# Kernel optimization log

Measured on AMD Instinct MI355X. Metric: run time of the kernel, lower is better.

## Reference

```python
import jax, jax.numpy as jnp
import numpy as np

BN_EPS = 1e-5
BN_SCALE = 1.0 / np.sqrt(1.0 + BN_EPS).astype(np.float32)  # running_mean=0, running_var=1


def _conv1x1(x, w, b=None):
    y = jnp.einsum('bchw,oc->bohw', x, w)
    if b is not None:
        y = y + b.reshape(1, -1, 1, 1)
    return y


def _bn(x, g, b):
    # eval-mode BN with running_mean=0, running_var=1
    return x * (BN_SCALE * g).reshape(1, -1, 1, 1) + b.reshape(1, -1, 1, 1)


def _spatial_attn(x, w, b):
    avg = jnp.mean(x, axis=1, keepdims=True)
    mx = jnp.max(x, axis=1, keepdims=True)
    s = jnp.concatenate([avg, mx], axis=1)  # [B,2,H,W]
    y = jax.lax.conv_general_dilated(s, w, (1, 1), [(3, 3), (3, 3)],
                                     dimension_numbers=('NCHW', 'OIHW', 'NCHW'))
    return jax.nn.sigmoid(y + b.reshape(1, -1, 1, 1))  # [B,1,H,W]


def _channel_attn(x, w1, b1, w2, b2):
    avg = jnp.mean(x, axis=(2, 3))  # [B,C]
    mx = jnp.max(x, axis=(2, 3))
    fc = lambda v: jax.nn.relu(v @ w1.T + b1) @ w2.T + b2
    return jax.nn.sigmoid(fc(avg) + fc(mx))[:, :, None, None]  # [B,C,1,1]


def setup_inputs() -> dict:
    key = jax.random.key(0)
    B, C, H, W = 8, 256, 48, 48
    Cr, Cm = C // 8, C // 16
    ks = iter(jax.random.split(key, 24))
    n = lambda shape, scale=0.05: jax.random.normal(next(ks), shape, jnp.float32) * scale
    return dict(
        rgb=jax.random.normal(next(ks), (B, C, H, W), jnp.float32),
        chm=jax.random.normal(next(ks), (B, C, H, W), jnp.float32),
        rgb_sa_w=n((1, 2, 7, 7)), rgb_sa_b=jnp.zeros((1,), jnp.float32),
        chm_sa_w=n((1, 2, 7, 7)), chm_sa_b=jnp.zeros((1,), jnp.float32),
        rgb_fc1_w=n((Cm, C)), rgb_fc1_b=jnp.zeros((Cm,), jnp.float32),
        rgb_fc2_w=n((C, Cm)), rgb_fc2_b=jnp.zeros((C,), jnp.float32),
        chm_fc1_w=n((Cm, C)), chm_fc1_b=jnp.zeros((Cm,), jnp.float32),
        chm_fc2_w=n((C, Cm)), chm_fc2_b=jnp.zeros((C,), jnp.float32),
        rq_w=n((Cr, C)), rq_b=jnp.zeros((Cr,), jnp.float32),
        rk_w=n((Cr, C)), rk_b=jnp.zeros((Cr,), jnp.float32),
        rv_w=n((C, C)), rv_b=jnp.zeros((C,), jnp.float32),
        dq_w=n((Cr, C)), dq_b=jnp.zeros((Cr,), jnp.float32),
        dk_w=n((Cr, C)), dk_b=jnp.zeros((Cr,), jnp.float32),
        dv_w=n((C, C)), dv_b=jnp.zeros((C,), jnp.float32),
        gate_w=n((C, 2 * C)), gate_b=jnp.zeros((C,), jnp.float32),
        mlp1_w=n((24, C)), mlp1_g=jnp.ones((24,), jnp.float32), mlp1_b=jnp.zeros((24,), jnp.float32),
        mlp2_w=n((1, 24)), mlp2_g=jnp.ones((1,), jnp.float32), mlp2_b=jnp.zeros((1,), jnp.float32),
    )


def reference(rgb, chm, rgb_sa_w, rgb_sa_b, chm_sa_w, chm_sa_b,
              rgb_fc1_w, rgb_fc1_b, rgb_fc2_w, rgb_fc2_b,
              chm_fc1_w, chm_fc1_b, chm_fc2_w, chm_fc2_b,
              rq_w, rq_b, rk_w, rk_b, rv_w, rv_b,
              dq_w, dq_b, dk_w, dk_b, dv_w, dv_b,
              gate_w, gate_b, mlp1_w, mlp1_g, mlp1_b, mlp2_w, mlp2_g, mlp2_b):
    B, C, H, W = rgb.shape
    N = H * W
    Cr = rq_w.shape[0]
    scale = Cr ** -0.5

    # channel / spatial attentions
    rgb_sa = _spatial_attn(rgb, rgb_sa_w, rgb_sa_b)
    chm_sa = _spatial_attn(chm, chm_sa_w, chm_sa_b)
    rgb_ca = _channel_attn(rgb, rgb_fc1_w, rgb_fc1_b, rgb_fc2_w, rgb_fc2_b)
    chm_ca = _channel_attn(chm, chm_fc1_w, chm_fc1_b, chm_fc2_w, chm_fc2_b)

    attn_rgb = rgb * chm_sa * chm_ca
    attn_chm = chm * rgb_sa * rgb_ca

    # CAWF dual cross-modal attention
    flat = lambda x: x.reshape(B, -1, N)
    rq = flat(_conv1x1(rgb, rq_w, rq_b))   # [B,Cr,N]
    rk = flat(_conv1x1(rgb, rk_w, rk_b))
    rv = flat(_conv1x1(rgb, rv_w, rv_b))   # [B,C,N]
    dq = flat(_conv1x1(chm, dq_w, dq_b))
    dk = flat(_conv1x1(chm, dk_w, dk_b))
    dv = flat(_conv1x1(chm, dv_w, dv_b))

    rgb_attn = jax.nn.softmax(jnp.einsum('bcn,bcm->bnm', rq, dk) * scale, axis=-1)  # [B,N,N]
    chm_attn = jax.nn.softmax(jnp.einsum('bcn,bcm->bnm', dq, rk) * scale, axis=-1)
    rgb_att = jnp.einsum('bcn,bnm->bcm', rv, rgb_attn).reshape(B, C, H, W)
    chm_att = jnp.einsum('bcn,bnm->bcm', dv, chm_attn).reshape(B, C, H, W)

    c = jnp.concatenate([rgb_att, chm_att], axis=1)
    g = jax.nn.sigmoid(_conv1x1(c, gate_w, gate_b))
    c_fused = rgb_att * g + chm_att * (1.0 - g)
    d_fused = rgb_att * chm_att
    output = c_fused + d_fused

    h = jax.nn.relu(_bn(_conv1x1(output, mlp1_w), mlp1_g, mlp1_b))
    h = jax.nn.sigmoid(_bn(_conv1x1(h, mlp2_w), mlp2_g, mlp2_b))
    weight = jax.nn.sigmoid(h)  # double sigmoid as in original mlp (ConvBNSig + nn.Sigmoid)

    return attn_rgb + attn_chm * weight
```

## Files before the change

### kernel.cpp

```cpp
#include <hip/hip_runtime.h>
#include <hip/hip_bf16.h>
#include <cstdint>

#define DI __device__ __forceinline__

typedef float f32x4 __attribute__((ext_vector_type(4)));
typedef short bf16x8 __attribute__((ext_vector_type(8)));
typedef unsigned short u16x4 __attribute__((ext_vector_type(4)));

constexpr int B_ = 8, C_ = 256, HH = 48, WW = 48, N_ = 2304, CR = 32;
constexpr float QK_SCALE = 0.17677669529663687f;
constexpr float BN_SC = 0.99999500003749968f;

constexpr size_t QK_SZ   = (size_t)B_*N_*CR*2;
constexpr size_t V_SZ    = (size_t)B_*C_*N_*2;
constexpr size_t OFF_RQT = 0;
constexpr size_t OFF_RKT = OFF_RQT + QK_SZ;
constexpr size_t OFF_DQT = OFF_RKT + QK_SZ;
constexpr size_t OFF_DKT = OFF_DQT + QK_SZ;
constexpr size_t OFF_RV  = OFF_DKT + QK_SZ;
constexpr size_t OFF_DV  = OFF_RV + V_SZ;
constexpr size_t OFF_ATT = OFF_DV + V_SZ;
constexpr size_t ATT_SZ  = 2ull*B_*C_*N_*2;
constexpr size_t OFF_PCS = OFF_ATT;
constexpr size_t OFF_PCM = OFF_ATT + 2ull*8*36*256*4;
constexpr size_t OFF_FUSED = OFF_RV;
constexpr size_t OFF_SCONV = OFF_ATT + ATT_SZ;
constexpr size_t SCONV_SZ  = 2ull*B_*2*N_*4;
constexpr size_t OFF_SA    = OFF_SCONV + SCONV_SZ;
constexpr size_t SA_SZ     = 2ull*B_*N_*4;
constexpr size_t OFF_CAVG  = OFF_SA + SA_SZ;
constexpr size_t CST_SZ    = 2ull*B_*C_*4;
constexpr size_t OFF_CMAX  = OFF_CAVG + CST_SZ;
constexpr size_t OFF_CA    = OFF_CMAX + CST_SZ;
constexpr size_t OFF_WMAP  = OFF_CA + CST_SZ;
constexpr size_t OFF_WPROJ = OFF_WMAP + (size_t)B_*N_*4;
constexpr size_t WPROJ_SZ  = 2ull*320*256*2;
constexpr size_t OFF_WGATE = OFF_WPROJ + WPROJ_SZ;
constexpr size_t WS_NEEDED = OFF_WGATE + 256ull*512*2;

DI float bf2f(unsigned short u){ union{unsigned int i; float f;} v; v.i = ((unsigned int)u)<<16; return v.f; }
DI unsigned short f2bf(float f){ union{float f; unsigned int i;} v; v.f=f; unsigned int r = v.i + 0x7fffu + ((v.i>>16)&1u); return (unsigned short)(r>>16); }
DI float sigm(float x){ return 1.0f/(1.0f+__expf(-x)); }
DI u16x4 pk4(float p0, float p1, float p2, float p3){
  union { __hip_bfloat162 h[2]; u16x4 v; } u;
  u.h[0] = __float22bfloat162_rn(make_float2(p0, p1));
  u.h[1] = __float22bfloat162_rn(make_float2(p2, p3));
  return u.v;
}

__global__ void k_prep_w(const float* rq_w, const float* rk_w, const float* rv_w,
                         const float* dq_w, const float* dk_w, const float* dv_w,
                         const float* gate_w, unsigned short* wproj, unsigned short* wgate){
  int i = blockIdx.x*256 + threadIdx.x;
  if (i < 163840){
    int mod = i / 81920, r = (i >> 8) % 320, c = i & 255;
    const float* q = mod ? dq_w : rq_w;
    const float* k = mod ? dk_w : rk_w;
    const float* v = mod ? dv_w : rv_w;
    float val = (r < 32) ? q[r*256+c] : (r < 64 ? k[(r-32)*256+c] : v[(r-64)*256+c]);
    wproj[i] = f2bf(val);
  } else {
    int j = i - 163840;
    if (j < 131072) wgate[j] = f2bf(gate_w[j]);
  }
}

__global__ __launch_bounds__(256, 2) void k_redfuse(const float* rgb, const float* chm,
                                                    float* sconv, float* pcs, float* pcm){
  int mod = blockIdx.y;
  int b = blockIdx.x / 36, nt = blockIdx.x % 36;
  int pix0 = nt*64;
  const float* X = (mod ? chm : rgb) + (size_t)b*C_*N_ + pix0;
  __shared__ float xt[128][65];
  __shared__ float ls[4][64], lm[4][64];
  int t = threadIdx.x;
  int p = t & 63, cg = t >> 6;
  int srow0 = t >> 4, scol = (t & 15)*4;
  float s = 0.f, mx = -INFINITY;
  float* pcsb = pcs + ((size_t)(mod*8+b)*36 + nt)*256;
  float* pcmb = pcm + ((size_t)(mod*8+b)*36 + nt)*256;
  for (int half = 0; half < 2; ++half){
    __syncthreads();
    #pragma unroll
    for (int rr = 0; rr < 8; ++rr){
      int row = rr*16 + srow0;
      float4 v = *(const float4*)(X + (size_t)(half*128 + row)*N_ + scol);
      xt[row][scol] = v.x; xt[row][scol+1] = v.y; xt[row][scol+2] = v.z; xt[row][scol+3] = v.w;
    }
    __syncthreads();
    #pragma unroll 8
    for (int cc = 0; cc < 32; ++cc){
      float v = xt[cg*32 + cc][p];
      s += v; mx = fmaxf(mx, v);
    }
    if (t < 128){
      float cs = 0.f, cm = -INFINITY;
      #pragma unroll 8
      for (int pp = 0; pp < 64; ++pp){
        float v = xt[t][pp];
        cs += v; cm = fmaxf(cm, v);
      }
      pcsb[half*128 + t] = cs;
      pcmb[half*128 + t] = cm;
    }
  }
  ls[cg][p] = s; lm[cg][p] = mx;
  __syncthreads();
  if (cg == 0){
    s = ls[0][p]+ls[1][p]+ls[2][p]+ls[3][p];
    mx = fmaxf(fmaxf(lm[0][p],lm[1][p]), fmaxf(lm[2][p],lm[3][p]));
    sconv[((size_t)(mod*B_+b)*2 + 0)*N_ + pix0+p] = s*(1.f/256.f);
    sconv[((size_t)(mod*B_+b)*2 + 1)*N_ + pix0+p] = mx;
  }
}

__global__ void k_red_combine(const float* pcs, const float* pcm, float* cavg, float* cmax){
  int mod = blockIdx.x >> 3, b = blockIdx.x & 7, c = threadIdx.x;
  float s = 0.f, mx = -INFINITY;
  for (int nt = 0; nt < 36; ++nt){
    s += pcs[((size_t)(mod*8+b)*36 + nt)*256 + c];
    mx = fmaxf(mx, pcm[((size_t)(mod*8+b)*36 + nt)*256 + c]);
  }
  cavg[(mod*B_+b)*C_ + c] = s*(1.f/(float)N_);
  cmax[(mod*B_+b)*C_ + c] = mx;
}

__global__ void k_sa_ca(const float* sconv, const float* rgb_sa_w, const float* rgb_sa_b,
                        const float* chm_sa_w, const float* chm_sa_b, float* sa,
                        const float* cavg, const float* cmax,
                        const float* rw1, const float* rb1, const float* rw2, const float* rb2,
                        const float* cw1, const float* cb1, const float* cw2, const float* cb2,
                        float* ca){
  int x = blockIdx.x;
  if (x < 144){
    int mod = x / 72;
    int idx = (x % 72)*256 + threadIdx.x;
    int b = idx / N_, pix = idx % N_;
    int y = pix / WW, xx0 = pix % WW;
    const float* w7 = mod ? chm_sa_w : rgb_sa_w;
    float acc = (mod ? chm_sa_b : rgb_sa_b)[0];
    const float* sin0 = sconv + (size_t)(mod*B_+b)*2*N_;
    #pragma unroll
    for (int ic = 0; ic < 2; ++ic)
      for (int ky = 0; ky < 7; ++ky){
        int yy = y + ky - 3; if (yy < 0 || yy >= HH) continue;
        for (int kx = 0; kx < 7; ++kx){
          int xx = xx0 + kx - 3; if (xx < 0 || xx >= WW) continue;
          acc += w7[(ic*7+ky)*7+kx] * sin0[ic*N_ + yy*WW + xx];
        }
      }
    sa[(mod*B_+b)*N_ + pix] = sigm(acc);
  } else {
    int y = x - 144;
    int mod = y >> 3, b = y & 7;
    const float* w1 = mod ? cw1 : rw1;  const float* b1 = mod ? cb1 : rb1;
    const float* w2 = mod ? cw2 : rw2;  const float* b2 = mod ? cb2 : rb2;
    __shared__ float va[256], vm[256], h1a[16], h1m[16];
    int t = threadIdx.x;
    va[t] = cavg[(mod*B_+b)*C_ + t];
    vm[t] = cmax[(mod*B_+b)*C_ + t];
    __syncthreads();
    if (t < 32){
      int j = t & 15;
      const float* v = (t >= 16) ? vm : va;
      float s = b1[j];
      for (int c = 0; c < 256; ++c) s += w1[j*256+c]*v[c];
      float* hp = (t >= 16) ? h1m : h1a;
      hp[j] = fmaxf(s, 0.f);
    }
    __syncthreads();
    float fa = b2[t], fm = b2[t];
    #pragma unroll
    for (int j = 0; j < 16; ++j){ fa += w2[t*16+j]*h1a[j]; fm += w2[t*16+j]*h1m[j]; }
    ca[(mod*B_+b)*C_ + t] = sigm(fa + fm);
  }
}

__global__ __launch_bounds__(256, 2) void k_proj(
                       const float* rgb, const float* chm, const unsigned short* wproj,
                       const float* rq_b, const float* rk_b, const float* rv_b,
                       const float* dq_b, const float* dk_b, const float* dv_b,
                       unsigned short* wsu){
  int mod = blockIdx.z, b = blockIdx.y;
  int pix0 = blockIdx.x * 64;
  const float* X = (mod ? chm : rgb) + (size_t)b*C_*N_;
  const unsigned short* Wm = wproj + (size_t)mod*320*256;
  int lane = threadIdx.x & 63, w = threadIdx.x >> 6;
  int l15 = lane & 15, g = lane >> 4;
  __shared__ unsigned short xs[32*68];
  int srow = threadIdx.x >> 3, scol = (threadIdx.x & 7)*8;
  f32x4 acc[5][4];
  #pragma unroll
  for (int i = 0; i < 5; ++i)
    #pragma unroll
    for (int j = 0; j < 4; ++j) acc[i][j] = 0.f;
  for (int k0 = 0; k0 < 256; k0 += 32){
    const float* sp = X + (size_t)(k0 + srow)*N_ + pix0 + scol;
    float4 v0 = *(const float4*)sp;
    float4 v1 = *(const float4*)(sp + 4);
    u16x4 h0 = { f2bf(v0.x), f2bf(v0.y), f2bf(v0.z), f2bf(v0.w) };
    u16x4 h1 = { f2bf(v1.x), f2bf(v1.y), f2bf(v1.z), f2bf(v1.w) };
    __syncthreads();
    *(u16x4*)(xs + srow*68 + scol) = h0;
    *(u16x4*)(xs + srow*68 + scol + 4) = h1;
    __syncthreads();
    bf16x8 af[5];
    #pragma unroll
    for (int cf = 0; cf < 5; ++cf)
      af[cf] = *(const bf16x8*)(Wm + (size_t)(w*80 + cf*16 + l15)*256 + k0 + g*8);
    bf16x8 bx[4];
    #pragma unroll
    for (int mf = 0; mf < 4; ++mf)
      #pragma unroll
      for (int j = 0; j < 8; ++j)
        bx[mf][j] = (short)xs[(g*8+j)*68 + mf*16 + l15];
    #pragma unroll
    for (int cf = 0; cf < 5; ++cf)
      #pragma unroll
      for (int mf = 0; mf < 4; ++mf)
        acc[cf][mf] = __builtin_amdgcn_mfma_f32_16x16x32_bf16(af[cf], bx[mf], acc[cf][mf], 0, 0, 0);
  }
  const float* qb = mod ? dq_b : rq_b;
  const float* kb = mod ? dk_b : rk_b;
  const float* vb = mod ? dv_b : rv_b;
  unsigned short* qT = wsu + (mod ? OFF_DQT : OFF_RQT)/2;
  unsigned short* kT = wsu + (mod ? OFF_DKT : OFF_RKT)/2;
  unsigned short* vB = wsu + (mod ? OFF_DV  : OFF_RV )/2;
  #pragma unroll
  for (int cf = 0; cf < 5; ++cf){
    int base = w*80 + cf*16;
    #pragma unroll
    for (int mf = 0; mf < 4; ++mf){
      int col = pix0 + mf*16 + l15;
      if (base < 32){
        int o4 = base + g*4;
        u16x4 pk = { f2bf(acc[cf][mf][0] + qb[o4]),   f2bf(acc[cf][mf][1] + qb[o4+1]),
                     f2bf(acc[cf][mf][2] + qb[o4+2]), f2bf(acc[cf][mf][3] + qb[o4+3]) };
        *(u16x4*)(qT + (size_t)(b*N_ + col)*32 + o4) = pk;
      } else if (base < 64){
        int o4 = base - 32 + g*4;
        u16x4 pk = { f2bf(acc[cf][mf][0] + kb[o4]),   f2bf(acc[cf][mf][1] + kb[o4+1]),
                     f2bf(acc[cf][mf][2] + kb[o4+2]), f2bf(acc[cf][mf][3] + kb[o4+3]) };
        *(u16x4*)(kT + (size_t)(b*N_ + col)*32 + o4) = pk;
      } else {
        #pragma unroll
        for (int r = 0; r < 4; ++r){
          int o = base - 64 + g*4 + r;
          vB[((size_t)b*C_ + o)*N_ + col] = f2bf(acc[cf][mf][r] + vb[o]);
        }
      }
    }
  }
}

__global__ void k_phase_a(unsigned short* wsu){
  int orig = blockIdx.x;
  int b = orig & 7;
  int logical = orig >> 3;
  int a = logical / 36;
  int nb0 = (logical % 36)*64;
  int lane = threadIdx.x & 63, w = threadIdx.x >> 6;
  int l15 = lane & 15, g = lane >> 4;
  int n0 = nb0 + w*16;
  const unsigned short* Q = wsu + (a ? OFF_DQT : OFF_RQT)/2;
  const unsigned short* K = wsu + (a ? OFF_RKT : OFF_DKT)/2;
  bf16x8 af = *(const bf16x8*)(Q + (size_t)(b*N_ + n0 + l15)*32 + g*8);
  float lrun[4] = {0.f,0.f,0.f,0.f};
  for (int m0 = 0; m0 < N_; m0 += 64){
    f32x4 d[4];
    #pragma unroll
    for (int s = 0; s < 4; ++s){
      bf16x8 bk = *(const bf16x8*)(K + (size_t)(b*N_ + m0 + s*16 + l15)*32 + g*8);
      f32x4 z = 0.f;
      d[s] = __builtin_amdgcn_mfma_f32_16x16x32_bf16(af, bk, z, 0, 0, 0);
    }
    #pragma unroll
    for (int r = 0; r < 4; ++r)
      lrun[r] += (__expf(d[0][r]*QK_SCALE)+__expf(d[1][r]*QK_SCALE))
               + (__expf(d[2][r]*QK_SCALE)+__expf(d[3][r]*QK_SCALE));
  }
  #pragma unroll
  for (int r = 0; r < 4; ++r)
    #pragma unroll
    for (int msk = 1; msk < 16; msk <<= 1) lrun[r] += __shfl_xor(lrun[r], msk);
  __shared__ float lsv[64];
  if (l15 == 0){
    #pragma unroll
    for (int r = 0; r < 4; ++r) lsv[w*16 + g*4 + r] = 1.0f / lrun[r];
  }
  __syncthreads();
  unsigned short* V = wsu + (a ? OFF_DV : OFF_RV)/2 + ((size_t)b*C_ + threadIdx.x)*N_ + nb0;
  #pragma unroll
  for (int j8 = 0; j8 < 8; ++j8){
    bf16x8 vv = *(const bf16x8*)(V + j8*8);
    bf16x8 ov;
    #pragma unroll
    for (int e = 0; e < 8; ++e)
      ov[e] = (short)f2bf(bf2f((unsigned short)vv[e]) * lsv[j8*8 + e]);
    *(bf16x8*)(V + j8*8) = ov;
  }
}

__global__ __launch_bounds__(256, 3) void k_pv5(
                          const unsigned short* wsu, unsigned short* att){
  int orig = blockIdx.x;
  int logical = (orig & 7)*72 + (orig >> 3);
  int pair = logical / 36, mblk = logical % 36;
  int a = pair >> 3, b = pair & 7;
  int m0 = mblk*64;
  int lane = threadIdx.x & 63, w = threadIdx.x >> 6;
  int l15 = lane & 15, g = lane >> 4;
  int qm  = (w & 1)*32;
  int qnn = (w >> 1)*64;
  const unsigned short* Q = wsu + (a ? OFF_DQT : OFF_RQT)/2;
  const unsigned short* K = wsu + (a ? OFF_RKT : OFF_DKT)/2;
  const unsigned short* V = wsu + (a ? OFF_DV  : OFF_RV )/2;
  __shared__ __align__(16) unsigned char plds[2][64*256];

  bf16x8 kb[2];
  #pragma unroll
  for (int s = 0; s < 2; ++s)
    kb[s] = *(const bf16x8*)(K + (size_t)(b*N_ + m0 + qm + s*16 + l15)*32 + g*8);

  f32x4 acc[4][4];
  #pragma unroll
  for (int i = 0; i < 4; ++i)
    #pragma unroll
    for (int j = 0; j < 4; ++j) acc[i][j] = 0.f;

  auto computePh = [&](int n0base, int buf, int half){
    #pragma unroll
    for (int fi = 0; fi < 2; ++fi){
      int fr = half*2 + fi;
      int nb = n0base + qnn + fr*16;
      bf16x8 qa = *(const bf16x8*)(Q + (size_t)(b*N_ + nb + l15)*32 + g*8);
      #pragma unroll
      for (int fm = 0; fm < 2; ++fm){
        f32x4 z = 0.f;
        f32x4 d = __builtin_amdgcn_mfma_f32_16x16x32_bf16(qa, kb[fm], z, 0, 0, 0);
        int ml = qm + fm*16 + l15;
        int nl = qnn + fr*16 + g*4;
        u16x4 pk = pk4(__expf(d[0]*QK_SCALE), __expf(d[1]*QK_SCALE),
                       __expf(d[2]*QK_SCALE), __expf(d[3]*QK_SCALE));
        *(u16x4*)(plds[buf] + ml*256 + ((nl*2) ^ ((ml&7)<<4))) = pk;
      }
    }
  };

  computePh(0, 0, 0);
  computePh(0, 0, 1);
  __syncthreads();
  for (int t = 0; t < 18; ++t){
    int n0 = t*128;
    const unsigned char* pbuf = plds[t & 1];
    #pragma unroll
    for (int s = 0; s < 4; ++s){
      bf16x8 pb[4];
      #pragma unroll
      for (int mf = 0; mf < 4; ++mf){
        int ml = mf*16 + l15;
        pb[mf] = *(const bf16x8*)(pbuf + ml*256 + ((s*64 + g*16) ^ ((ml&7)<<4)));
      }
      bf16x8 av[4];
      #pragma unroll
      for (int cf = 0; cf < 4; ++cf)
        av[cf] = *(const bf16x8*)(V + ((size_t)b*C_ + w*64 + cf*16 + l15)*N_ + n0 + s*32 + g*8);
      if (t < 17 && s < 2) computePh(n0 + 128, (t+1)&1, s);
      __builtin_amdgcn_s_setprio(1);
      #pragma unroll
      for (int cf = 0; cf < 4; ++cf)
        #pragma unroll
        for (int mf = 0; mf < 4; ++mf)
          acc[cf][mf] = __builtin_amdgcn_mfma_f32_16x16x32_bf16(av[cf], pb[mf], acc[cf][mf], 0, 0, 0);
      __builtin_amdgcn_s_setprio(0);
    }
    __syncthreads();
  }
  unsigned short* ap = att + (((size_t)a*8 + b)*256)*N_;
  #pragma unroll
  for (int cf = 0; cf < 4; ++cf)
    #pragma unroll
    for (int mf = 0; mf < 4; ++mf)
      #pragma unroll
      for (int r = 0; r < 4; ++r){
        int c = w*64 + cf*16 + g*4 + r;
        int m = m0 + mf*16 + l15;
        ap[(size_t)c*N_ + m] = f2bf(acc[cf][mf][r]);
      }
}

__global__ __launch_bounds__(256, 2) void k_gatefuse(
                           const unsigned short* att, const unsigned short* wgate,
                           const float* gate_b, unsigned short* fused){
  int b = blockIdx.y, m0 = blockIdx.x*32;
  int lane = threadIdx.x & 63, w = threadIdx.x >> 6;
  int l15 = lane & 15, g = lane >> 4;
  __shared__ unsigned short ats[32][520];
  int row8 = threadIdx.x >> 3;
  int mq = (threadIdx.x & 7)*4;
  for (int rb = 0; rb < 16; ++rb){
    int k = rb*32 + row8;
    int aa = k >> 8, c = k & 255;
    size_t base = (((size_t)aa*8 + b)*256 + c)*N_ + m0 + mq;
    u16x4 p0 = *(const u16x4*)(att + base);
    #pragma unroll
    for (int j = 0; j < 4; ++j) ats[mq + j][k] = p0[j];
  }
  __syncthreads();
  f32x4 acc[4][2];
  #pragma unroll
  for (int i = 0; i < 4; ++i){ acc[i][0] = 0.f; acc[i][1] = 0.f; }
  for (int k0 = 0; k0 < 512; k0 += 32){
    bf16x8 aw[4], bt[2];
    #pragma unroll
    for (int of = 0; of < 4; ++of)
      aw[of] = *(const bf16x8*)(wgate + (size_t)(w*64 + of*16 + l15)*512 + k0 + g*8);
    #pragma unroll
    for (int mf = 0; mf < 2; ++mf)
      bt[mf] = *(const bf16x8*)(&ats[mf*16 + l15][k0 + g*8]);
    #pragma unroll
    for (int of = 0; of < 4; ++of)
      #pragma unroll
      for (int mf = 0; mf < 2; ++mf)
        acc[of][mf] = __builtin_amdgcn_mfma_f32_16x16x32_bf16(aw[of], bt[mf], acc[of][mf], 0, 0, 0);
  }
  #pragma unroll
  for (int of = 0; of < 4; ++of){
    int o4 = w*64 + of*16 + g*4;
    float4 gb4 = *(const float4*)(gate_b + o4);
    #pragma unroll
    for (int mf = 0; mf < 2; ++mf){
      int ml = mf*16 + l15;
      int m = m0 + ml;
      u16x4 ra4 = *(const u16x4*)(&ats[ml][o4]);
      u16x4 da4 = *(const u16x4*)(&ats[ml][256 + o4]);
      #pragma unroll
      for (int r = 0; r < 4; ++r){
        float gg = sigm(acc[of][mf][r] + (&gb4.x)[r]);
        float ra = bf2f(ra4[r]);
        float da = bf2f(da4[r]);
        float fv = ra*gg + da*(1.f - gg) + ra*da;
        fused[((size_t)b*C_ + o4 + r)*N_ + m] = f2bf(fv);
      }
    }
  }
}

__global__ void k_mlp(const unsigned short* fused, const float* w1, const float* g1, const float* b1,
                      const float* w2, const float* g2, const float* b2, float* wmap){
  int b = blockIdx.x / 36, pix0 = (blockIdx.x % 36)*64;
  __shared__ unsigned short ft[256*64];
  __shared__ float hs[24][64];
  const unsigned short* F = fused + (size_t)b*C_*N_ + pix0;
  int c0 = threadIdx.x >> 3, l8 = threadIdx.x & 7;
  for (int cc = 0; cc < 256; cc += 32)
    *(bf16x8*)(ft + (size_t)(cc + c0)*64 + l8*8) = *(const bf16x8*)(F + (size_t)(cc + c0)*N_ + l8*8);
  __syncthreads();
  int p = threadIdx.x & 63, jg = threadIdx.x >> 6;
  float h[6] = {0.f,0.f,0.f,0.f,0.f,0.f};
  for (int c = 0; c < 256; ++c){
    float v = bf2f(ft[c*64 + p]);
    #pragma unroll
    for (int jj = 0; jj < 6; ++jj) h[jj] += w1[(jg*6+jj)*256 + c] * v;
  }
  #pragma unroll
  for (int jj = 0; jj < 6; ++jj) hs[jg*6+jj][p] = h[jj];
  __syncthreads();
  if (threadIdx.x < 64){
    int pp = threadIdx.x;
    float s2 = 0.f;
    #pragma unroll
    for (int j = 0; j < 24; ++j){
      float hj = fmaxf(hs[j][pp]*(BN_SC*g1[j]) + b1[j], 0.f);
      s2 += w2[j]*hj;
    }
    s2 = s2*(BN_SC*g2[0]) + b2[0];
    wmap[b*N_ + pix0 + pp] = sigm(sigm(s2));
  }
}

__global__ void k_final(const float* rgb, const float* chm, const float* sa, const float* ca,
                        const float* wmap, float* out){
  const int total4 = B_*C_*N_/4;
  for (int i = blockIdx.x*blockDim.x + threadIdx.x; i < total4; i += gridDim.x*blockDim.x){
    int e = i*4;
    int b = e / (C_*N_);
    int rem = e % (C_*N_);
    int c = rem / N_;
    int pix = rem % N_;
    float4 rv = *(const float4*)(rgb + e);
    float4 cv = *(const float4*)(chm + e);
    float4 sc = *(const float4*)(sa + (size_t)(B_ + b)*N_ + pix);
    float4 sr = *(const float4*)(sa + (size_t)b*N_ + pix);
    float4 wm = *(const float4*)(wmap + (size_t)b*N_ + pix);
    float cac = ca[(B_ + b)*C_ + c];
    float car = ca[b*C_ + c];
    float4 o;
    o.x = rv.x*sc.x*cac + cv.x*sr.x*car*wm.x;
    o.y = rv.y*sc.y*cac + cv.y*sr.y*car*wm.y;
    o.z = rv.z*sc.z*cac + cv.z*sr.z*car*wm.z;
    o.w = rv.w*sc.w*cac + cv.w*sr.w*car*wm.w;
    *(float4*)(out + e) = o;
  }
}

extern "C" void kernel_launch(void* const* d_in, const int* in_sizes, int n_in,
                              void* d_out, int out_size, void* d_ws, size_t ws_size,
                              hipStream_t stream){
  if (ws_size < WS_NEEDED) return;
  const float* rgb      = (const float*)d_in[0];
  const float* chm      = (const float*)d_in[1];
  const float* rgb_sa_w = (const float*)d_in[2];
  const float* rgb_sa_b = (const float*)d_in[3];
  const float* chm_sa_w = (const float*)d_in[4];
  const float* chm_sa_b = (const float*)d_in[5];
  const float* rgb_fc1_w= (const float*)d_in[6];
  const float* rgb_fc1_b= (const float*)d_in[7];
  const float* rgb_fc2_w= (const float*)d_in[8];
  const float* rgb_fc2_b= (const float*)d_in[9];
  const float* chm_fc1_w= (const float*)d_in[10];
  const float* chm_fc1_b= (const float*)d_in[11];
  const float* chm_fc2_w= (const float*)d_in[12];
  const float* chm_fc2_b= (const float*)d_in[13];
  const float* rq_w = (const float*)d_in[14];
  const float* rq_b = (const float*)d_in[15];
  const float* rk_w = (const float*)d_in[16];
  const float* rk_b = (const float*)d_in[17];
  const float* rv_w = (const float*)d_in[18];
  const float* rv_b = (const float*)d_in[19];
  const float* dq_w = (const float*)d_in[20];
  const float* dq_b = (const float*)d_in[21];
  const float* dk_w = (const float*)d_in[22];
  const float* dk_b = (const float*)d_in[23];
  const float* dv_w = (const float*)d_in[24];
  const float* dv_b = (const float*)d_in[25];
  const float* gate_w = (const float*)d_in[26];
  const float* gate_b = (const float*)d_in[27];
  const float* mlp1_w = (const float*)d_in[28];
  const float* mlp1_g = (const float*)d_in[29];
  const float* mlp1_b = (const float*)d_in[30];
  const float* mlp2_w = (const float*)d_in[31];
  const float* mlp2_g = (const float*)d_in[32];
  const float* mlp2_b = (const float*)d_in[33];

  char* ws = (char*)d_ws;
  unsigned short* wsu   = (unsigned short*)d_ws;
  float* sconv = (float*)(ws + OFF_SCONV);
  float* sa    = (float*)(ws + OFF_SA);
  float* cavg  = (float*)(ws + OFF_CAVG);
  float* cmax  = (float*)(ws + OFF_CMAX);
  float* ca    = (float*)(ws + OFF_CA);
  float* wmap  = (float*)(ws + OFF_WMAP);
  float* pcs   = (float*)(ws + OFF_PCS);
  float* pcm   = (float*)(ws + OFF_PCM);
  unsigned short* wproj = (unsigned short*)(ws + OFF_WPROJ);
  unsigned short* wgate = (unsigned short*)(ws + OFF_WGATE);
  unsigned short* att   = (unsigned short*)(ws + OFF_ATT);
  unsigned short* fused = (unsigned short*)(ws + OFF_FUSED);

  k_prep_w<<<dim3(1152), dim3(256), 0, stream>>>(rq_w, rk_w, rv_w, dq_w, dk_w, dv_w, gate_w, wproj, wgate);
  k_redfuse<<<dim3(288,2), dim3(256), 0, stream>>>(rgb, chm, sconv, pcs, pcm);
  k_red_combine<<<dim3(16), dim3(256), 0, stream>>>(pcs, pcm, cavg, cmax);
  k_sa_ca<<<dim3(160), dim3(256), 0, stream>>>(sconv, rgb_sa_w, rgb_sa_b, chm_sa_w, chm_sa_b, sa,
                                               cavg, cmax, rgb_fc1_w, rgb_fc1_b, rgb_fc2_w, rgb_fc2_b,
                                               chm_fc1_w, chm_fc1_b, chm_fc2_w, chm_fc2_b, ca);
  k_proj<<<dim3(36,8,2), dim3(256), 0, stream>>>(rgb, chm, wproj, rq_b, rk_b, rv_b, dq_b, dk_b, dv_b, wsu);
  k_phase_a<<<dim3(576), dim3(256), 0, stream>>>(wsu);
  k_pv5<<<dim3(576), dim3(256), 0, stream>>>(wsu, att);
  k_gatefuse<<<dim3(72,8), dim3(256), 0, stream>>>(att, wgate, gate_b, fused);
  k_mlp<<<dim3(288), dim3(256), 0, stream>>>(fused, mlp1_w, mlp1_g, mlp1_b, mlp2_w, mlp2_g, mlp2_b, wmap);
  k_final<<<dim3(2048), dim3(256), 0, stream>>>(rgb, chm, sa, ca, wmap, (float*)d_out);
}
```

Baseline: 283.0 us.

## Halve PV tile to 32 columns, prefetch V fragments, fold channel reduce combine

The PV attention kernel now uses 32 output columns per block instead of 64. That doubles the grid to 1152 blocks, halves the LDS P buffer and raises the occupancy target to 4 blocks. V fragments are loaded one step ahead (register double buffering) so global-load latency overlaps the MFMAs, and the LDS swizzle is widened to match. Separately, the channel-stat combine kernel is folded into k_sa_ca, removing one launch. Smaller tiles mean each V row is read twice as often and QK exp work is duplicated per block, in exchange for better latency hiding and occupancy.

```diff
diff --git a/kernel.cpp b/kernel.cpp
--- a/kernel.cpp
+++ b/kernel.cpp
@@ -29,10 +29,8 @@
 constexpr size_t SCONV_SZ  = 2ull*B_*2*N_*4;
 constexpr size_t OFF_SA    = OFF_SCONV + SCONV_SZ;
 constexpr size_t SA_SZ     = 2ull*B_*N_*4;
-constexpr size_t OFF_CAVG  = OFF_SA + SA_SZ;
+constexpr size_t OFF_CA    = OFF_SA + SA_SZ;
 constexpr size_t CST_SZ    = 2ull*B_*C_*4;
-constexpr size_t OFF_CMAX  = OFF_CAVG + CST_SZ;
-constexpr size_t OFF_CA    = OFF_CMAX + CST_SZ;
 constexpr size_t OFF_WMAP  = OFF_CA + CST_SZ;
 constexpr size_t OFF_WPROJ = OFF_WMAP + (size_t)B_*N_*4;
 constexpr size_t WPROJ_SZ  = 2ull*320*256*2;
@@ -115,20 +113,9 @@
   }
 }
 
-__global__ void k_red_combine(const float* pcs, const float* pcm, float* cavg, float* cmax){
-  int mod = blockIdx.x >> 3, b = blockIdx.x & 7, c = threadIdx.x;
-  float s = 0.f, mx = -INFINITY;
-  for (int nt = 0; nt < 36; ++nt){
-    s += pcs[((size_t)(mod*8+b)*36 + nt)*256 + c];
-    mx = fmaxf(mx, pcm[((size_t)(mod*8+b)*36 + nt)*256 + c]);
-  }
-  cavg[(mod*B_+b)*C_ + c] = s*(1.f/(float)N_);
-  cmax[(mod*B_+b)*C_ + c] = mx;
-}
-
 __global__ void k_sa_ca(const float* sconv, const float* rgb_sa_w, const float* rgb_sa_b,
                         const float* chm_sa_w, const float* chm_sa_b, float* sa,
-                        const float* cavg, const float* cmax,
+                        const float* pcs, const float* pcm,
                         const float* rw1, const float* rb1, const float* rw2, const float* rb2,
                         const float* cw1, const float* cb1, const float* cw2, const float* cb2,
                         float* ca){
@@ -158,16 +145,21 @@
     const float* w2 = mod ? cw2 : rw2;  const float* b2 = mod ? cb2 : rb2;
     __shared__ float va[256], vm[256], h1a[16], h1m[16];
     int t = threadIdx.x;
-    va[t] = cavg[(mod*B_+b)*C_ + t];
-    vm[t] = cmax[(mod*B_+b)*C_ + t];
+    float s = 0.f, mx = -INFINITY;
+    for (int nt = 0; nt < 36; ++nt){
+      s += pcs[((size_t)(mod*8+b)*36 + nt)*256 + t];
+      mx = fmaxf(mx, pcm[((size_t)(mod*8+b)*36 + nt)*256 + t]);
+    }
+    va[t] = s*(1.f/(float)N_);
+    vm[t] = mx;
     __syncthreads();
     if (t < 32){
       int j = t & 15;
       const float* v = (t >= 16) ? vm : va;
-      float s = b1[j];
-      for (int c = 0; c < 256; ++c) s += w1[j*256+c]*v[c];
+      float ss = b1[j];
+      for (int c = 0; c < 256; ++c) ss += w1[j*256+c]*v[c];
       float* hp = (t >= 16) ? h1m : h1a;
-      hp[j] = fmaxf(s, 0.f);
+      hp[j] = fmaxf(ss, 0.f);
     }
     __syncthreads();
     float fa = b2[t], fm = b2[t];
@@ -302,51 +294,46 @@
   }
 }
 
-__global__ __launch_bounds__(256, 3) void k_pv5(
+__global__ __launch_bounds__(256, 4) void k_pv6(
                           const unsigned short* wsu, unsigned short* att){
   int orig = blockIdx.x;
-  int logical = (orig & 7)*72 + (orig >> 3);
-  int pair = logical / 36, mblk = logical % 36;
+  int logical = (orig & 7)*144 + (orig >> 3);
+  int pair = logical / 72, mblk = logical % 72;
   int a = pair >> 3, b = pair & 7;
-  int m0 = mblk*64;
+  int m0 = mblk*32;
   int lane = threadIdx.x & 63, w = threadIdx.x >> 6;
   int l15 = lane & 15, g = lane >> 4;
-  int qm  = (w & 1)*32;
-  int qnn = (w >> 1)*64;
+  int qnn = w*32;
   const unsigned short* Q = wsu + (a ? OFF_DQT : OFF_RQT)/2;
   const unsigned short* K = wsu + (a ? OFF_RKT : OFF_DKT)/2;
   const unsigned short* V = wsu + (a ? OFF_DV  : OFF_RV )/2;
-  __shared__ __align__(16) unsigned char plds[2][64*256];
+  __shared__ __align__(16) unsigned char plds[2][32*256];
 
   bf16x8 kb[2];
   #pragma unroll
   for (int s = 0; s < 2; ++s)
-    kb[s] = *(const bf16x8*)(K + (size_t)(b*N_ + m0 + qm + s*16 + l15)*32 + g*8);
-
-  f32x4 acc[4][4];
-  #pragma unroll
-  for (int i = 0; i < 4; ++i)
-    #pragma unroll
-    for (int j = 0; j < 4; ++j) acc[i][j] = 0.f;
+    kb[s] = *(const bf16x8*)(K + (size_t)(b*N_ + m0 + s*16 + l15)*32 + g*8);
+
+  f32x4 acc[4][2];
+  #pragma unroll
+  for (int i = 0; i < 4; ++i){ acc[i][0] = 0.f; acc[i][1] = 0.f; }
 
   auto computePh = [&](int n0base, int buf, int half){
-    #pragma unroll
-    for (int fi = 0; fi < 2; ++fi){
-      int fr = half*2 + fi;
-      int nb = n0base + qnn + fr*16;
-      bf16x8 qa = *(const bf16x8*)(Q + (size_t)(b*N_ + nb + l15)*32 + g*8);
-      #pragma unroll
-      for (int fm = 0; fm < 2; ++fm){
-        f32x4 z = 0.f;
-        f32x4 d = __builtin_amdgcn_mfma_f32_16x16x32_bf16(qa, kb[fm], z, 0, 0, 0);
-        int ml = qm + fm*16 + l15;
-        int nl = qnn + fr*16 + g*4;
-        u16x4 pk = pk4(__expf(d[0]*QK_SCALE), __expf(d[1]*QK_SCALE),
-                       __expf(d[2]*QK_SCALE), __expf(d[3]*QK_SCALE));
-        *(u16x4*)(plds[buf] + ml*256 + ((nl*2) ^ ((ml&7)<<4))) = pk;
-      }
+    int nb = n0base + qnn + half*16;
+    bf16x8 qa = *(const bf16x8*)(Q + (size_t)(b*N_ + nb + l15)*32 + g*8);
+    #pragma unroll
+    for (int fm = 0; fm < 2; ++fm){
+      f32x4 z = 0.f;
+      f32x4 d = __builtin_amdgcn_mfma_f32_16x16x32_bf16(qa, kb[fm], z, 0, 0, 0);
+      int ml = fm*16 + l15;
+      int nl = qnn + half*16 + g*4;
+      u16x4 pk = pk4(__expf(d[0]*QK_SCALE), __expf(d[1]*QK_SCALE),
+                     __expf(d[2]*QK_SCALE), __expf(d[3]*QK_SCALE));
+      *(u16x4*)(plds[buf] + ml*256 + ((nl*2) ^ ((ml&15)<<4))) = pk;
     }
   };
+
+  const unsigned short* Vb = V + ((size_t)b*C_ + w*64 + l15)*N_;
 
   computePh(0, 0, 0);
   computePh(0, 0, 1);
@@ -354,26 +341,35 @@
   for (int t = 0; t < 18; ++t){
     int n0 = t*128;
     const unsigned char* pbuf = plds[t & 1];
+    bf16x8 av[4], avn[4];
+    #pragma unroll
+    for (int cf = 0; cf < 4; ++cf)
+      av[cf] = *(const bf16x8*)(Vb + (size_t)cf*16*N_ + n0 + g*8);
     #pragma unroll
     for (int s = 0; s < 4; ++s){
-      bf16x8 pb[4];
-      #pragma unroll
-      for (int mf = 0; mf < 4; ++mf){
+      bf16x8 pb[2];
+      #pragma unroll
+      for (int mf = 0; mf < 2; ++mf){
         int ml = mf*16 + l15;
-        pb[mf] = *(const bf16x8*)(pbuf + ml*256 + ((s*64 + g*16) ^ ((ml&7)<<4)));
-      }
-      bf16x8 av[4];
-      #pragma unroll
-      for (int cf = 0; cf < 4; ++cf)
-        av[cf] = *(const bf16x8*)(V + ((size_t)b*C_ + w*64 + cf*16 + l15)*N_ + n0 + s*32 + g*8);
+        pb[mf] = *(const bf16x8*)(pbuf + ml*256 + ((s*64 + g*16) ^ ((ml&15)<<4)));
+      }
+      if (s < 3){
+        #pragma unroll
+        for (int cf = 0; cf < 4; ++cf)
+          avn[cf] = *(const bf16x8*)(Vb + (size_t)cf*16*N_ + n0 + (s+1)*32 + g*8);
+      }
       if (t < 17 && s < 2) computePh(n0 + 128, (t+1)&1, s);
       __builtin_amdgcn_s_setprio(1);
       #pragma unroll
       for (int cf = 0; cf < 4; ++cf)
         #pragma unroll
-        for (int mf = 0; mf < 4; ++mf)
+        for (int mf = 0; mf < 2; ++mf)
           acc[cf][mf] = __builtin_amdgcn_mfma_f32_16x16x32_bf16(av[cf], pb[mf], acc[cf][mf], 0, 0, 0);
       __builtin_amdgcn_s_setprio(0);
+      if (s < 3){
+        #pragma unroll
+        for (int cf = 0; cf < 4; ++cf) av[cf] = avn[cf];
+      }
     }
     __syncthreads();
   }
@@ -381,7 +377,7 @@
   #pragma unroll
   for (int cf = 0; cf < 4; ++cf)
     #pragma unroll
-    for (int mf = 0; mf < 4; ++mf)
+    for (int mf = 0; mf < 2; ++mf)
       #pragma unroll
       for (int r = 0; r < 4; ++r){
         int c = w*64 + cf*16 + g*4 + r;
@@ -548,8 +544,6 @@
   unsigned short* wsu   = (unsigned short*)d_ws;
   float* sconv = (float*)(ws + OFF_SCONV);
   float* sa    = (float*)(ws + OFF_SA);
-  float* cavg  = (float*)(ws + OFF_CAVG);
-  float* cmax  = (float*)(ws + OFF_CMAX);
   float* ca    = (float*)(ws + OFF_CA);
   float* wmap  = (float*)(ws + OFF_WMAP);
   float* pcs   = (float*)(ws + OFF_PCS);
@@ -561,13 +555,12 @@
 
   k_prep_w<<<dim3(1152), dim3(256), 0, stream>>>(rq_w, rk_w, rv_w, dq_w, dk_w, dv_w, gate_w, wproj, wgate);
   k_redfuse<<<dim3(288,2), dim3(256), 0, stream>>>(rgb, chm, sconv, pcs, pcm);
-  k_red_combine<<<dim3(16), dim3(256), 0, stream>>>(pcs, pcm, cavg, cmax);
   k_sa_ca<<<dim3(160), dim3(256), 0, stream>>>(sconv, rgb_sa_w, rgb_sa_b, chm_sa_w, chm_sa_b, sa,
-                                               cavg, cmax, rgb_fc1_w, rgb_fc1_b, rgb_fc2_w, rgb_fc2_b,
+                                               pcs, pcm, rgb_fc1_w, rgb_fc1_b, rgb_fc2_w, rgb_fc2_b,
                                                chm_fc1_w, chm_fc1_b, chm_fc2_w, chm_fc2_b, ca);
   k_proj<<<dim3(36,8,2), dim3(256), 0, stream>>>(rgb, chm, wproj, rq_b, rk_b, rv_b, dq_b, dk_b, dv_b, wsu);
   k_phase_a<<<dim3(576), dim3(256), 0, stream>>>(wsu);
-  k_pv5<<<dim3(576), dim3(256), 0, stream>>>(wsu, att);
+  k_pv6<<<dim3(1152), dim3(256), 0, stream>>>(wsu, att);
   k_gatefuse<<<dim3(72,8), dim3(256), 0, stream>>>(att, wgate, gate_b, fused);
   k_mlp<<<dim3(288), dim3(256), 0, stream>>>(fused, mlp1_w, mlp1_g, mlp1_b, mlp2_w, mlp2_g, mlp2_b, wmap);
   k_final<<<dim3(2048), dim3(256), 0, stream>>>(rgb, chm, sa, ca, wmap, (float*)d_out);
```

Result: slower. 337.7 us (+19.4%).

## Fuse input reductions into projection, fold combine into attention gates, fuse gate+MLP

Applied to the files above, without the earlier changes.

The spatial/channel reduction kernel and the QKV projection kernel are merged. Each block loads its full 256-channel by 64-pixel input tile once into shared memory as bf16, computes the reductions, then runs the MFMA projection from the same tile. This removes a second full read of rgb/chm. The per-tile channel partials are now combined inside k_sa_ca, which drops one launch. The gate-fuse and MLP kernels are also merged so the fused activation stays in shared memory instead of being written to and re-read from global memory. As a side effect, the mean and max statistics are now computed from bf16-rounded inputs, which slightly changes numerics.

```diff
diff --git a/kernel.cpp b/kernel.cpp
--- a/kernel.cpp
+++ b/kernel.cpp
@@ -24,15 +24,12 @@
 constexpr size_t ATT_SZ  = 2ull*B_*C_*N_*2;
 constexpr size_t OFF_PCS = OFF_ATT;
 constexpr size_t OFF_PCM = OFF_ATT + 2ull*8*36*256*4;
-constexpr size_t OFF_FUSED = OFF_RV;
 constexpr size_t OFF_SCONV = OFF_ATT + ATT_SZ;
 constexpr size_t SCONV_SZ  = 2ull*B_*2*N_*4;
 constexpr size_t OFF_SA    = OFF_SCONV + SCONV_SZ;
 constexpr size_t SA_SZ     = 2ull*B_*N_*4;
-constexpr size_t OFF_CAVG  = OFF_SA + SA_SZ;
+constexpr size_t OFF_CA    = OFF_SA + SA_SZ;
 constexpr size_t CST_SZ    = 2ull*B_*C_*4;
-constexpr size_t OFF_CMAX  = OFF_CAVG + CST_SZ;
-constexpr size_t OFF_CA    = OFF_CMAX + CST_SZ;
 constexpr size_t OFF_WMAP  = OFF_CA + CST_SZ;
 constexpr size_t OFF_WPROJ = OFF_WMAP + (size_t)B_*N_*4;
 constexpr size_t WPROJ_SZ  = 2ull*320*256*2;
@@ -66,145 +63,65 @@
   }
 }
 
-__global__ __launch_bounds__(256, 2) void k_redfuse(const float* rgb, const float* chm,
-                                                    float* sconv, float* pcs, float* pcm){
+__global__ __launch_bounds__(256, 2) void k_stage(
+                       const float* rgb, const float* chm, const unsigned short* wproj,
+                       const float* rq_b, const float* rk_b, const float* rv_b,
+                       const float* dq_b, const float* dk_b, const float* dv_b,
+                       unsigned short* wsu, float* sconv, float* pcs, float* pcm){
   int mod = blockIdx.y;
   int b = blockIdx.x / 36, nt = blockIdx.x % 36;
   int pix0 = nt*64;
   const float* X = (mod ? chm : rgb) + (size_t)b*C_*N_ + pix0;
-  __shared__ float xt[128][65];
+  __shared__ unsigned short xs[256*68];
   __shared__ float ls[4][64], lm[4][64];
   int t = threadIdx.x;
-  int p = t & 63, cg = t >> 6;
-  int srow0 = t >> 4, scol = (t & 15)*4;
-  float s = 0.f, mx = -INFINITY;
-  float* pcsb = pcs + ((size_t)(mod*8+b)*36 + nt)*256;
-  float* pcmb = pcm + ((size_t)(mod*8+b)*36 + nt)*256;
-  for (int half = 0; half < 2; ++half){
-    __syncthreads();
-    #pragma unroll
-    for (int rr = 0; rr < 8; ++rr){
-      int row = rr*16 + srow0;
-      float4 v = *(const float4*)(X + (size_t)(half*128 + row)*N_ + scol);
-      xt[row][scol] = v.x; xt[row][scol+1] = v.y; xt[row][scol+2] = v.z; xt[row][scol+3] = v.w;
-    }
-    __syncthreads();
-    #pragma unroll 8
-    for (int cc = 0; cc < 32; ++cc){
-      float v = xt[cg*32 + cc][p];
+  {
+    int srow = t >> 4;
+    int scol = (t & 15) * 4;
+    #pragma unroll
+    for (int rr = 0; rr < 16; ++rr){
+      int row = rr*16 + srow;
+      float4 v = *(const float4*)(X + (size_t)row*N_ + scol);
+      u16x4 h = { f2bf(v.x), f2bf(v.y), f2bf(v.z), f2bf(v.w) };
+      *(u16x4*)(xs + row*68 + scol) = h;
+    }
+  }
+  __syncthreads();
+  {
+    int p = t & 63, cg = t >> 6;
+    float s = 0.f, mx = -INFINITY;
+    for (int cc = 0; cc < 64; ++cc){
+      float v = bf2f(xs[(cg*64+cc)*68 + p]);
       s += v; mx = fmaxf(mx, v);
     }
-    if (t < 128){
-      float cs = 0.f, cm = -INFINITY;
-      #pragma unroll 8
-      for (int pp = 0; pp < 64; ++pp){
-        float v = xt[t][pp];
-        cs += v; cm = fmaxf(cm, v);
-      }
-      pcsb[half*128 + t] = cs;
-      pcmb[half*128 + t] = cm;
-    }
-  }
-  ls[cg][p] = s; lm[cg][p] = mx;
-  __syncthreads();
-  if (cg == 0){
-    s = ls[0][p]+ls[1][p]+ls[2][p]+ls[3][p];
-    mx = fmaxf(fmaxf(lm[0][p],lm[1][p]), fmaxf(lm[2][p],lm[3][p]));
+    ls[cg][p] = s; lm[cg][p] = mx;
+  }
+  {
+    float cs = 0.f, cm = -INFINITY;
+    for (int p = 0; p < 64; ++p){
+      float v = bf2f(xs[t*68 + p]);
+      cs += v; cm = fmaxf(cm, v);
+    }
+    pcs[((size_t)(mod*8+b)*36 + nt)*256 + t] = cs;
+    pcm[((size_t)(mod*8+b)*36 + nt)*256 + t] = cm;
+  }
+  __syncthreads();
+  if (t < 64){
+    int p = t;
+    float s = ls[0][p]+ls[1][p]+ls[2][p]+ls[3][p];
+    float mx = fmaxf(fmaxf(lm[0][p],lm[1][p]), fmaxf(lm[2][p],lm[3][p]));
     sconv[((size_t)(mod*B_+b)*2 + 0)*N_ + pix0+p] = s*(1.f/256.f);
     sconv[((size_t)(mod*B_+b)*2 + 1)*N_ + pix0+p] = mx;
   }
-}
-
-__global__ void k_red_combine(const float* pcs, const float* pcm, float* cavg, float* cmax){
-  int mod = blockIdx.x >> 3, b = blockIdx.x & 7, c = threadIdx.x;
-  float s = 0.f, mx = -INFINITY;
-  for (int nt = 0; nt < 36; ++nt){
-    s += pcs[((size_t)(mod*8+b)*36 + nt)*256 + c];
-    mx = fmaxf(mx, pcm[((size_t)(mod*8+b)*36 + nt)*256 + c]);
-  }
-  cavg[(mod*B_+b)*C_ + c] = s*(1.f/(float)N_);
-  cmax[(mod*B_+b)*C_ + c] = mx;
-}
-
-__global__ void k_sa_ca(const float* sconv, const float* rgb_sa_w, const float* rgb_sa_b,
-                        const float* chm_sa_w, const float* chm_sa_b, float* sa,
-                        const float* cavg, const float* cmax,
-                        const float* rw1, const float* rb1, const float* rw2, const float* rb2,
-                        const float* cw1, const float* cb1, const float* cw2, const float* cb2,
-                        float* ca){
-  int x = blockIdx.x;
-  if (x < 144){
-    int mod = x / 72;
-    int idx = (x % 72)*256 + threadIdx.x;
-    int b = idx / N_, pix = idx % N_;
-    int y = pix / WW, xx0 = pix % WW;
-    const float* w7 = mod ? chm_sa_w : rgb_sa_w;
-    float acc = (mod ? chm_sa_b : rgb_sa_b)[0];
-    const float* sin0 = sconv + (size_t)(mod*B_+b)*2*N_;
-    #pragma unroll
-    for (int ic = 0; ic < 2; ++ic)
-      for (int ky = 0; ky < 7; ++ky){
-        int yy = y + ky - 3; if (yy < 0 || yy >= HH) continue;
-        for (int kx = 0; kx < 7; ++kx){
-          int xx = xx0 + kx - 3; if (xx < 0 || xx >= WW) continue;
-          acc += w7[(ic*7+ky)*7+kx] * sin0[ic*N_ + yy*WW + xx];
-        }
-      }
-    sa[(mod*B_+b)*N_ + pix] = sigm(acc);
-  } else {
-    int y = x - 144;
-    int mod = y >> 3, b = y & 7;
-    const float* w1 = mod ? cw1 : rw1;  const float* b1 = mod ? cb1 : rb1;
-    const float* w2 = mod ? cw2 : rw2;  const float* b2 = mod ? cb2 : rb2;
-    __shared__ float va[256], vm[256], h1a[16], h1m[16];
-    int t = threadIdx.x;
-    va[t] = cavg[(mod*B_+b)*C_ + t];
-    vm[t] = cmax[(mod*B_+b)*C_ + t];
-    __syncthreads();
-    if (t < 32){
-      int j = t & 15;
-      const float* v = (t >= 16) ? vm : va;
-      float s = b1[j];
-      for (int c = 0; c < 256; ++c) s += w1[j*256+c]*v[c];
-      float* hp = (t >= 16) ? h1m : h1a;
-      hp[j] = fmaxf(s, 0.f);
-    }
-    __syncthreads();
-    float fa = b2[t], fm = b2[t];
-    #pragma unroll
-    for (int j = 0; j < 16; ++j){ fa += w2[t*16+j]*h1a[j]; fm += w2[t*16+j]*h1m[j]; }
-    ca[(mod*B_+b)*C_ + t] = sigm(fa + fm);
-  }
-}
-
-__global__ __launch_bounds__(256, 2) void k_proj(
-                       const float* rgb, const float* chm, const unsigned short* wproj,
-                       const float* rq_b, const float* rk_b, const float* rv_b,
-                       const float* dq_b, const float* dk_b, const float* dv_b,
-                       unsigned short* wsu){
-  int mod = blockIdx.z, b = blockIdx.y;
-  int pix0 = blockIdx.x * 64;
-  const float* X = (mod ? chm : rgb) + (size_t)b*C_*N_;
   const unsigned short* Wm = wproj + (size_t)mod*320*256;
-  int lane = threadIdx.x & 63, w = threadIdx.x >> 6;
+  int lane = t & 63, w = t >> 6;
   int l15 = lane & 15, g = lane >> 4;
-  __shared__ unsigned short xs[32*68];
-  int srow = threadIdx.x >> 3, scol = (threadIdx.x & 7)*8;
   f32x4 acc[5][4];
   #pragma unroll
   for (int i = 0; i < 5; ++i)
     #pragma unroll
     for (int j = 0; j < 4; ++j) acc[i][j] = 0.f;
   for (int k0 = 0; k0 < 256; k0 += 32){
-    const float* sp = X + (size_t)(k0 + srow)*N_ + pix0 + scol;
-    float4 v0 = *(const float4*)sp;
-    float4 v1 = *(const float4*)(sp + 4);
-    u16x4 h0 = { f2bf(v0.x), f2bf(v0.y), f2bf(v0.z), f2bf(v0.w) };
-    u16x4 h1 = { f2bf(v1.x), f2bf(v1.y), f2bf(v1.z), f2bf(v1.w) };
-    __syncthreads();
-    *(u16x4*)(xs + srow*68 + scol) = h0;
-    *(u16x4*)(xs + srow*68 + scol + 4) = h1;
-    __syncthreads();
     bf16x8 af[5];
     #pragma unroll
     for (int cf = 0; cf < 5; ++cf)
@@ -214,7 +131,7 @@
     for (int mf = 0; mf < 4; ++mf)
       #pragma unroll
       for (int j = 0; j < 8; ++j)
-        bx[mf][j] = (short)xs[(g*8+j)*68 + mf*16 + l15];
+        bx[mf][j] = (short)xs[(k0 + g*8 + j)*68 + mf*16 + l15];
     #pragma unroll
     for (int cf = 0; cf < 5; ++cf)
       #pragma unroll
@@ -254,6 +171,62 @@
   }
 }
 
+__global__ void k_sa_ca(const float* sconv, const float* rgb_sa_w, const float* rgb_sa_b,
+                        const float* chm_sa_w, const float* chm_sa_b, float* sa,
+                        const float* pcs, const float* pcm,
+                        const float* rw1, const float* rb1, const float* rw2, const float* rb2,
+                        const float* cw1, const float* cb1, const float* cw2, const float* cb2,
+                        float* ca){
+  int x = blockIdx.x;
+  if (x < 144){
+    int mod = x / 72;
+    int idx = (x % 72)*256 + threadIdx.x;
+    int b = idx / N_, pix = idx % N_;
+    int y = pix / WW, xx0 = pix % WW;
+    const float* w7 = mod ? chm_sa_w : rgb_sa_w;
+    float acc = (mod ? chm_sa_b : rgb_sa_b)[0];
+    const float* sin0 = sconv + (size_t)(mod*B_+b)*2*N_;
+    #pragma unroll
+    for (int ic = 0; ic < 2; ++ic)
+      for (int ky = 0; ky < 7; ++ky){
+        int yy = y + ky - 3; if (yy < 0 || yy >= HH) continue;
+        for (int kx = 0; kx < 7; ++kx){
+          int xx = xx0 + kx - 3; if (xx < 0 || xx >= WW) continue;
+          acc += w7[(ic*7+ky)*7+kx] * sin0[ic*N_ + yy*WW + xx];
+        }
+      }
+    sa[(mod*B_+b)*N_ + pix] = sigm(acc);
+  } else {
+    int y = x - 144;
+    int mod = y >> 3, b = y & 7;
+    const float* w1 = mod ? cw1 : rw1;  const float* b1 = mod ? cb1 : rb1;
+    const float* w2 = mod ? cw2 : rw2;  const float* b2 = mod ? cb2 : rb2;
+    __shared__ float va[256], vm[256], h1a[16], h1m[16];
+    int t = threadIdx.x;
+    float s = 0.f, mx = -INFINITY;
+    for (int nt = 0; nt < 36; ++nt){
+      s += pcs[((size_t)(mod*8+b)*36 + nt)*256 + t];
+      mx = fmaxf(mx, pcm[((size_t)(mod*8+b)*36 + nt)*256 + t]);
+    }
+    va[t] = s*(1.f/(float)N_);
+    vm[t] = mx;
+    __syncthreads();
+    if (t < 32){
+      int j = t & 15;
+      const float* v = (t >= 16) ? vm : va;
+      float ss = b1[j];
+      for (int c = 0; c < 256; ++c) ss += w1[j*256+c]*v[c];
+      float* hp = (t >= 16) ? h1m : h1a;
+      hp[j] = fmaxf(ss, 0.f);
+    }
+    __syncthreads();
+    float fa = b2[t], fm = b2[t];
+    #pragma unroll
+    for (int j = 0; j < 16; ++j){ fa += w2[t*16+j]*h1a[j]; fm += w2[t*16+j]*h1m[j]; }
+    ca[(mod*B_+b)*C_ + t] = sigm(fa + fm);
+  }
+}
+
 __global__ void k_phase_a(unsigned short* wsu){
   int orig = blockIdx.x;
   int b = orig & 7;
@@ -390,13 +363,18 @@
       }
 }
 
-__global__ __launch_bounds__(256, 2) void k_gatefuse(
+__global__ __launch_bounds__(256, 2) void k_gatemlp(
                            const unsigned short* att, const unsigned short* wgate,
-                           const float* gate_b, unsigned short* fused){
+                           const float* gate_b,
+                           const float* w1, const float* g1, const float* b1,
+                           const float* w2, const float* g2, const float* b2,
+                           float* wmap){
   int b = blockIdx.y, m0 = blockIdx.x*32;
   int lane = threadIdx.x & 63, w = threadIdx.x >> 6;
   int l15 = lane & 15, g = lane >> 4;
   __shared__ unsigned short ats[32][520];
+  __shared__ unsigned short fvs[256][34];
+  __shared__ float hs[24][33];
   int row8 = threadIdx.x >> 3;
   int mq = (threadIdx.x & 7)*4;
   for (int rb = 0; rb < 16; ++rb){
@@ -432,7 +410,6 @@
     #pragma unroll
     for (int mf = 0; mf < 2; ++mf){
       int ml = mf*16 + l15;
-      int m = m0 + ml;
       u16x4 ra4 = *(const u16x4*)(&ats[ml][o4]);
       u16x4 da4 = *(const u16x4*)(&ats[ml][256 + o4]);
       #pragma unroll
@@ -441,42 +418,34 @@
         float ra = bf2f(ra4[r]);
         float da = bf2f(da4[r]);
         float fv = ra*gg + da*(1.f - gg) + ra*da;
-        fused[((size_t)b*C_ + o4 + r)*N_ + m] = f2bf(fv);
+        fvs[o4 + r][ml] = f2bf(fv);
       }
     }
   }
-}
-
-__global__ void k_mlp(const unsigned short* fused, const float* w1, const float* g1, const float* b1,
-                      const float* w2, const float* g2, const float* b2, float* wmap){
-  int b = blockIdx.x / 36, pix0 = (blockIdx.x % 36)*64;
-  __shared__ unsigned short ft[256*64];
-  __shared__ float hs[24][64];
-  const unsigned short* F = fused + (size_t)b*C_*N_ + pix0;
-  int c0 = threadIdx.x >> 3, l8 = threadIdx.x & 7;
-  for (int cc = 0; cc < 256; cc += 32)
-    *(bf16x8*)(ft + (size_t)(cc + c0)*64 + l8*8) = *(const bf16x8*)(F + (size_t)(cc + c0)*N_ + l8*8);
-  __syncthreads();
-  int p = threadIdx.x & 63, jg = threadIdx.x >> 6;
-  float h[6] = {0.f,0.f,0.f,0.f,0.f,0.f};
-  for (int c = 0; c < 256; ++c){
-    float v = bf2f(ft[c*64 + p]);
-    #pragma unroll
-    for (int jj = 0; jj < 6; ++jj) h[jj] += w1[(jg*6+jj)*256 + c] * v;
-  }
-  #pragma unroll
-  for (int jj = 0; jj < 6; ++jj) hs[jg*6+jj][p] = h[jj];
-  __syncthreads();
-  if (threadIdx.x < 64){
-    int pp = threadIdx.x;
+  __syncthreads();
+  {
+    int m = threadIdx.x & 31, jg = threadIdx.x >> 5;
+    const float* w1r0 = w1 + (size_t)(jg*3+0)*256;
+    const float* w1r1 = w1 + (size_t)(jg*3+1)*256;
+    const float* w1r2 = w1 + (size_t)(jg*3+2)*256;
+    float h0 = 0.f, h1 = 0.f, h2 = 0.f;
+    for (int c = 0; c < 256; ++c){
+      float v = bf2f(fvs[c][m]);
+      h0 += w1r0[c]*v; h1 += w1r1[c]*v; h2 += w1r2[c]*v;
+    }
+    hs[jg*3+0][m] = h0; hs[jg*3+1][m] = h1; hs[jg*3+2][m] = h2;
+  }
+  __syncthreads();
+  if (threadIdx.x < 32){
+    int mm = threadIdx.x;
     float s2 = 0.f;
     #pragma unroll
     for (int j = 0; j < 24; ++j){
-      float hj = fmaxf(hs[j][pp]*(BN_SC*g1[j]) + b1[j], 0.f);
+      float hj = fmaxf(hs[j][mm]*(BN_SC*g1[j]) + b1[j], 0.f);
       s2 += w2[j]*hj;
     }
     s2 = s2*(BN_SC*g2[0]) + b2[0];
-    wmap[b*N_ + pix0 + pp] = sigm(sigm(s2));
+    wmap[b*N_ + m0 + mm] = sigm(sigm(s2));
   }
 }
 
@@ -548,8 +517,6 @@
   unsigned short* wsu   = (unsigned short*)d_ws;
   float* sconv = (float*)(ws + OFF_SCONV);
   float* sa    = (float*)(ws + OFF_SA);
-  float* cavg  = (float*)(ws + OFF_CAVG);
-  float* cmax  = (float*)(ws + OFF_CMAX);
   float* ca    = (float*)(ws + OFF_CA);
   float* wmap  = (float*)(ws + OFF_WMAP);
   float* pcs   = (float*)(ws + OFF_PCS);
@@ -557,18 +524,16 @@
   unsigned short* wproj = (unsigned short*)(ws + OFF_WPROJ);
   unsigned short* wgate = (unsigned short*)(ws + OFF_WGATE);
   unsigned short* att   = (unsigned short*)(ws + OFF_ATT);
-  unsigned short* fused = (unsigned short*)(ws + OFF_FUSED);
 
   k_prep_w<<<dim3(1152), dim3(256), 0, stream>>>(rq_w, rk_w, rv_w, dq_w, dk_w, dv_w, gate_w, wproj, wgate);
-  k_redfuse<<<dim3(288,2), dim3(256), 0, stream>>>(rgb, chm, sconv, pcs, pcm);
-  k_red_combine<<<dim3(16), dim3(256), 0, stream>>>(pcs, pcm, cavg, cmax);
+  k_stage<<<dim3(288,2), dim3(256), 0, stream>>>(rgb, chm, wproj, rq_b, rk_b, rv_b, dq_b, dk_b, dv_b,
+                                                 wsu, sconv, pcs, pcm);
   k_sa_ca<<<dim3(160), dim3(256), 0, stream>>>(sconv, rgb_sa_w, rgb_sa_b, chm_sa_w, chm_sa_b, sa,
-                                               cavg, cmax, rgb_fc1_w, rgb_fc1_b, rgb_fc2_w, rgb_fc2_b,
+                                               pcs, pcm, rgb_fc1_w, rgb_fc1_b, rgb_fc2_w, rgb_fc2_b,
                                                chm_fc1_w, chm_fc1_b, chm_fc2_w, chm_fc2_b, ca);
-  k_proj<<<dim3(36,8,2), dim3(256), 0, stream>>>(rgb, chm, wproj, rq_b, rk_b, rv_b, dq_b, dk_b, dv_b, wsu);
   k_phase_a<<<dim3(576), dim3(256), 0, stream>>>(wsu);
   k_pv5<<<dim3(576), dim3(256), 0, stream>>>(wsu, att);
-  k_gatefuse<<<dim3(72,8), dim3(256), 0, stream>>>(att, wgate, gate_b, fused);
-  k_mlp<<<dim3(288), dim3(256), 0, stream>>>(fused, mlp1_w, mlp1_g, mlp1_b, mlp2_w, mlp2_g, mlp2_b, wmap);
+  k_gatemlp<<<dim3(72,8), dim3(256), 0, stream>>>(att, wgate, gate_b,
+                                                  mlp1_w, mlp1_g, mlp1_b, mlp2_w, mlp2_g, mlp2_b, wmap);
   k_final<<<dim3(2048), dim3(256), 0, stream>>>(rgb, chm, sa, ca, wmap, (float*)d_out);
 }
```

After: 260.0 us. -8.1%, faster.
